# Kernel tuning notes

Measured on AMD Instinct MI355X. Metric: run time of the kernel, lower is better.

Reference implementation:

```python
import jax, jax.numpy as jnp
import numpy as np
from jax import lax

H = 32  # hidden size


def _lstm_layer(x, Wih, Whh, bih, bhh):
    """x: [B, T, D_in]; returns [B, T, H]. PyTorch gate order i,f,g,o."""
    B = x.shape[0]
    b = bih + bhh  # [4H]
    # precompute input projections for all timesteps: [T, B, 4H]
    xp = jnp.einsum('btd,gd->tbg', x, Wih) + b

    def step(carry, xt):
        h, c = carry
        gates = xt + h @ Whh.T  # [B, 4H]
        i, f, g, o = jnp.split(gates, 4, axis=-1)
        i = jax.nn.sigmoid(i)
        f = jax.nn.sigmoid(f)
        g = jnp.tanh(g)
        o = jax.nn.sigmoid(o)
        c = f * c + i * g
        h = o * jnp.tanh(c)
        return (h, c), h

    init = (jnp.zeros((B, H), x.dtype), jnp.zeros((B, H), x.dtype))
    _, ys = lax.scan(step, init, xp)  # ys: [T, B, H]
    return jnp.swapaxes(ys, 0, 1)


def _lstm5(x, Wih0, Wih_rest, Whh, bih, bhh):
    h = _lstm_layer(x, Wih0, Whh[0], bih[0], bhh[0])
    for l in range(4):  # fixed small layer count
        h = _lstm_layer(h, Wih_rest[l], Whh[l + 1], bih[l + 1], bhh[l + 1])
    return h


def setup_inputs() -> dict:
    key = jax.random.key(0)
    ks = jax.random.split(key, 18)
    s = 1.0 / np.sqrt(H)
    B, T = 16384, 20
    u = lambda k, shp: jax.random.uniform(k, shp, jnp.float32, -s, s)
    return {
        'accel': jax.random.normal(ks[0], (B, T, 3), jnp.float32),
        'gyro': jax.random.normal(ks[1], (B, T, 3), jnp.float32),
        'accel_Wih0': u(ks[2], (4 * H, 3)),
        'accel_Wih_rest': u(ks[3], (4, 4 * H, H)),
        'accel_Whh': u(ks[4], (5, 4 * H, H)),
        'accel_bih': u(ks[5], (5, 4 * H)),
        'accel_bhh': u(ks[6], (5, 4 * H)),
        'gyro_Wih0': u(ks[7], (4 * H, 3)),
        'gyro_Wih_rest': u(ks[8], (4, 4 * H, H)),
        'gyro_Whh': u(ks[9], (5, 4 * H, H)),
        'gyro_bih': u(ks[10], (5, 4 * H)),
        'gyro_bhh': u(ks[11], (5, 4 * H)),
        'fc1_w': u(ks[12], (128, T * H * 2)),
        'fc1_b': u(ks[13], (128,)),
        'fc2_w': u(ks[14], (5, 128)),
        'fc2_b': u(ks[15], (5,)),
    }


def reference(accel, gyro, accel_Wih0, accel_Wih_rest, accel_Whh, accel_bih,
              accel_bhh, gyro_Wih0, gyro_Wih_rest, gyro_Whh, gyro_bih,
              gyro_bhh, fc1_w, fc1_b, fc2_w, fc2_b):
    a = _lstm5(accel, accel_Wih0, accel_Wih_rest, accel_Whh, accel_bih, accel_bhh)
    g = _lstm5(gyro, gyro_Wih0, gyro_Wih_rest, gyro_Whh, gyro_bih, gyro_bhh)
    x = jnp.concatenate([a, g], axis=1)          # [B, 2T, H]
    x = x.reshape(x.shape[0], -1)                # [B, 2*T*H]
    x = jax.nn.relu(x @ fc1_w.T + fc1_b)         # [B, 128]
    return x @ fc2_w.T + fc2_b                   # [B, 5]
```

## Files before the change

kernel.cpp:

```cpp
#include <hip/hip_runtime.h>
#include <math.h>

#define B_TOTAL 16384
#define T_STEPS 20
#define NGRP    1024

typedef __attribute__((ext_vector_type(8))) __bf16 bf16x8;
typedef __attribute__((ext_vector_type(4))) float f32x4;

__device__ __forceinline__ __bf16 bf16_bits(unsigned short s) {
    __bf16 r; __builtin_memcpy(&r, &s, 2); return r;
}
__device__ __forceinline__ void split_trunc(float x, __bf16& hi, __bf16& lo) {
    unsigned u = __float_as_uint(x);
    hi = bf16_bits((unsigned short)(u >> 16));
    float l = x - __uint_as_float(u & 0xFFFF0000u);
    lo = bf16_bits((unsigned short)(__float_as_uint(l) >> 16));
}

__device__ __forceinline__ float lstm_act(f32x4 a, float& c) {
    float eA = __expf(-a[0]);
    float eB = __expf(-a[1]);
    float eC = __expf(2.0f * a[2]);
    float aA = 1.0f + eA, aB = 1.0f + eB, aC = 1.0f + eC;
    float pAC = aA * aC;
    float r1  = __builtin_amdgcn_rcpf(pAC * aB);
    c = fmaf(c, pAC, (eC - 1.0f) * aB) * r1;
    float eD = __expf(-a[3]);
    float eE = __expf(2.0f * c);
    float r2 = __builtin_amdgcn_rcpf((1.0f + eD) * (1.0f + eE));
    return (eE - 1.0f) * r2;
}

__global__ __launch_bounds__(512, 8)
void lstm5_mfma(const float* __restrict__ accel, const float* __restrict__ gyro,
                const float* __restrict__ aWih0, const float* __restrict__ aWihR,
                const float* __restrict__ aWhh,  const float* __restrict__ aBih,
                const float* __restrict__ aBhh,
                const float* __restrict__ gWih0, const float* __restrict__ gWihR,
                const float* __restrict__ gWhh,  const float* __restrict__ gBih,
                const float* __restrict__ gBhh,
                __bf16* __restrict__ Xhi, __bf16* __restrict__ Xlo) {
    const int tid  = threadIdx.x;
    const int w    = tid >> 6;
    const int lane = tid & 63;
    const int e    = lane & 15;
    const int quad = lane >> 4;
    const int sensor = blockIdx.y;
    const int bbase  = blockIdx.x * 16;

    const float* xin  = sensor ? gyro  : accel;
    const float* Wih0 = sensor ? gWih0 : aWih0;
    const float* WihR = sensor ? gWihR : aWihR;
    const float* Whh  = sensor ? gWhh  : aWhh;
    const float* Bih  = sensor ? gBih  : aBih;
    const float* Bhh  = sensor ? gBhh  : aBhh;

    __shared__ __align__(16) __bf16 shi[20 * 512];
    __shared__ __align__(16) __bf16 slo[20 * 512];

    const int ug  = w * 4 + quad;
    const int swz = (e >> 1) & 3;

    const int widx = (e * 16 + ((w * 2 + (quad >> 1)) ^ (swz << 2))) * 2 + (quad & 1);
    const int rb_base = e * 32 + ((quad ^ swz) << 3);

    const int m_row = lane & 15;
    const int orow  = (m_row & 3) * 32 + (w * 4 + (m_row >> 2));

    bf16x8 wih_h, wih_l, whh_h, whh_l;
    f32x4  biasv;
    float  c0 = 0.f;

#define LOAD_FRAG(Wsrc, fh, fl)                               \
    {                                                         \
        const float* p_ = (Wsrc) + (orow) * 32 + quad * 8;    \
        _Pragma("unroll")                                     \
        for (int jj = 0; jj < 8; ++jj) {                      \
            __bf16 h_, l_;                                    \
            split_trunc(p_[jj], h_, l_);                      \
            (fh)[jj] = h_;  (fl)[jj] = l_;                    \
        }                                                     \
    }

#define LOAD_BIAS(l)                                                        \
    {                                                                       \
        _Pragma("unroll")                                                   \
        for (int r = 0; r < 4; ++r)                                         \
            biasv[r] = Bih[(l) * 128 + r * 32 + ug] + Bhh[(l) * 128 + r * 32 + ug]; \
    }

#define ACT_STORE(t)                                                        \
    {                                                                       \
        float h0 = lstm_act(acc, c0);                                       \
        __bf16 hh_, ll_;                                                    \
        split_trunc(h0, hh_, ll_);                                          \
        __syncthreads();             \
        shi[(t) * 512 + widx] = hh_;                                        \
        slo[(t) * 512 + widx] = ll_;                                        \
        __syncthreads();       \
    }

    {
        LOAD_FRAG(Whh, whh_h, whh_l);
        LOAD_BIAS(0);
        float w0reg[4][3];
#pragma unroll
        for (int r = 0; r < 4; ++r)
#pragma unroll
            for (int k = 0; k < 3; ++k)
                w0reg[r][k] = Wih0[(r * 32 + ug) * 3 + k];
        const float* xrow = xin + (size_t)(bbase + e) * (T_STEPS * 3);

        for (int t = 0; t < T_STEPS; ++t) {
            float x0 = xrow[t * 3 + 0];
            float x1 = xrow[t * 3 + 1];
            float x2 = xrow[t * 3 + 2];
            f32x4 acc = biasv;
#pragma unroll
            for (int r = 0; r < 4; ++r)
                acc[r] = fmaf(w0reg[r][0], x0,
                         fmaf(w0reg[r][1], x1,
                         fmaf(w0reg[r][2], x2, acc[r])));
            if (t > 0) {
                int rb = (t - 1) * 512 + rb_base;
                bf16x8 bh = *(const bf16x8*)&shi[rb];
                bf16x8 bl = *(const bf16x8*)&slo[rb];
                acc = __builtin_amdgcn_mfma_f32_16x16x32_bf16(whh_h, bh, acc, 0, 0, 0);
                acc = __builtin_amdgcn_mfma_f32_16x16x32_bf16(whh_h, bl, acc, 0, 0, 0);
                acc = __builtin_amdgcn_mfma_f32_16x16x32_bf16(whh_l, bh, acc, 0, 0, 0);
            }
            ACT_STORE(t);
        }
    }

    for (int l = 1; l < 5; ++l) {
        const float* Wi = WihR + (l - 1) * 4096;
        const float* Wh = Whh + l * 4096;
        LOAD_FRAG(Wi, wih_h, wih_l);
        LOAD_FRAG(Wh, whh_h, whh_l);
        LOAD_BIAS(l);
        c0 = 0.f;

        for (int t = 0; t < T_STEPS; ++t) {
            const int rb1 = t * 512 + rb_base;
            bf16x8 bh1 = *(const bf16x8*)&shi[rb1];
            bf16x8 bl1 = *(const bf16x8*)&slo[rb1];
            f32x4 acc;
            acc = __builtin_amdgcn_mfma_f32_16x16x32_bf16(wih_h, bh1, biasv, 0, 0, 0);
            acc = __builtin_amdgcn_mfma_f32_16x16x32_bf16(wih_h, bl1, acc, 0, 0, 0);
            acc = __builtin_amdgcn_mfma_f32_16x16x32_bf16(wih_l, bh1, acc, 0, 0, 0);
            if (t > 0) {
                const int rb0 = rb1 - 512;
                bf16x8 bh = *(const bf16x8*)&shi[rb0];
                bf16x8 bl = *(const bf16x8*)&slo[rb0];
                acc = __builtin_amdgcn_mfma_f32_16x16x32_bf16(whh_h, bh, acc, 0, 0, 0);
                acc = __builtin_amdgcn_mfma_f32_16x16x32_bf16(whh_h, bl, acc, 0, 0, 0);
                acc = __builtin_amdgcn_mfma_f32_16x16x32_bf16(whh_l, bh, acc, 0, 0, 0);
            }
            ACT_STORE(t);
        }
    }
    __syncthreads();

    {
        size_t base = ((size_t)(sensor * NGRP + blockIdx.x)) * (20 * 512);
        float4* dh = (float4*)(Xhi + base);
        float4* dl = (float4*)(Xlo + base);
        const float4* sh = (const float4*)shi;
        const float4* sl = (const float4*)slo;
        for (int i = tid; i < 1280; i += 512) { dh[i] = sh[i]; dl[i] = sl[i]; }
    }
#undef LOAD_FRAG
#undef LOAD_BIAS
#undef ACT_STORE
}

__global__ void w1_prep(const float* __restrict__ w1,
                        __bf16* __restrict__ w1ah, __bf16* __restrict__ w1al) {
    int t = blockIdx.x * blockDim.x + threadIdx.x;
    if (t >= 20480) return;
    int lane = t & 63;
    int ks   = (t >> 6) % 40;
    int mt   = t / (64 * 40);
    int row  = mt * 16 + (lane & 15);
    int col0 = ks * 32 + (lane >> 4) * 8;
    const float* src = w1 + row * 1280 + col0;
#pragma unroll
    for (int j = 0; j < 8; ++j) {
        __bf16 h_, l_;
        split_trunc(src[j], h_, l_);
        w1ah[t * 8 + j] = h_;
        w1al[t * 8 + j] = l_;
    }
}

__global__ __launch_bounds__(256, 4)
void fc_mfma(const __bf16* __restrict__ Xhi, const __bf16* __restrict__ Xlo,
             const __bf16* __restrict__ w1ah, const __bf16* __restrict__ w1al,
             const float* __restrict__ fc1_b, const float* __restrict__ fc2_w,
             const float* __restrict__ fc2_b, float* __restrict__ out) {
    const int tid  = threadIdx.x;
    const int wv   = tid >> 6;
    const int lane = tid & 63;
    const int e    = lane & 15;
    const int quad = lane >> 4;
    const int g    = blockIdx.x;

    const int lnoff = e * 32 + ((quad ^ ((e >> 1) & 3)) << 3);

    __shared__ __align__(16) f32x4 sacc[4][8][64];
    __shared__ float sred[4][16][5];

    f32x4 acc[8];
#pragma unroll
    for (int m = 0; m < 8; ++m) acc[m] = (f32x4){0.f, 0.f, 0.f, 0.f};

    for (int kk = 0; kk < 10; ++kk) {
        int ks = wv * 10 + kk;
        int sensor = ks / 20, t = ks % 20;
        size_t bb = ((size_t)(sensor * NGRP + g)) * (20 * 512) + t * 512 + lnoff;
        bf16x8 bh = *(const bf16x8*)(Xhi + bb);
        bf16x8 bl = *(const bf16x8*)(Xlo + bb);
#pragma unroll
        for (int m = 0; m < 8; ++m) {
            const __bf16* ap = w1ah + ((size_t)((m * 40 + ks) * 64 + lane)) * 8;
            const __bf16* al = w1al + ((size_t)((m * 40 + ks) * 64 + lane)) * 8;
            bf16x8 ah = *(const bf16x8*)ap;
            bf16x8 av = *(const bf16x8*)al;
            acc[m] = __builtin_amdgcn_mfma_f32_16x16x32_bf16(ah, bh, acc[m], 0, 0, 0);
            acc[m] = __builtin_amdgcn_mfma_f32_16x16x32_bf16(ah, bl, acc[m], 0, 0, 0);
            acc[m] = __builtin_amdgcn_mfma_f32_16x16x32_bf16(av, bh, acc[m], 0, 0, 0);
        }
    }
#pragma unroll
    for (int m = 0; m < 8; ++m) sacc[wv][m][lane] = acc[m];
    __syncthreads();

    float p[5] = {0.f, 0.f, 0.f, 0.f, 0.f};
#pragma unroll
    for (int mm = 0; mm < 2; ++mm) {
        int mt = wv * 2 + mm;
        f32x4 z = sacc[0][mt][lane];
#pragma unroll
        for (int k = 1; k < 4; ++k) {
            f32x4 zz = sacc[k][mt][lane];
#pragma unroll
            for (int r = 0; r < 4; ++r) z[r] += zz[r];
        }
#pragma unroll
        for (int r = 0; r < 4; ++r) {
            int row = mt * 16 + quad * 4 + r;
            float v = fmaxf(z[r] + fc1_b[row], 0.f);
#pragma unroll
            for (int n = 0; n < 5; ++n) p[n] = fmaf(v, fc2_w[n * 128 + row], p[n]);
        }
    }
#pragma unroll
    for (int n = 0; n < 5; ++n) {
        p[n] += __shfl_xor(p[n], 16, 64);
        p[n] += __shfl_xor(p[n], 32, 64);
    }
    if (quad == 0) {
#pragma unroll
        for (int n = 0; n < 5; ++n) sred[wv][e][n] = p[n];
    }
    __syncthreads();
    if (tid < 80) {
        int col = tid / 5, n = tid - col * 5;
        out[(size_t)(g * 16 + col) * 5 + n] =
            sred[0][col][n] + sred[1][col][n] + sred[2][col][n] + sred[3][col][n] + fc2_b[n];
    }
}

extern "C" void kernel_launch(void* const* d_in, const int* in_sizes, int n_in,
                              void* d_out, int out_size, void* d_ws, size_t ws_size,
                              hipStream_t stream) {
    const float* accel  = (const float*)d_in[0];
    const float* gyro   = (const float*)d_in[1];
    const float* aWih0  = (const float*)d_in[2];
    const float* aWihR  = (const float*)d_in[3];
    const float* aWhh   = (const float*)d_in[4];
    const float* aBih   = (const float*)d_in[5];
    const float* aBhh   = (const float*)d_in[6];
    const float* gWih0  = (const float*)d_in[7];
    const float* gWihR  = (const float*)d_in[8];
    const float* gWhh   = (const float*)d_in[9];
    const float* gBih   = (const float*)d_in[10];
    const float* gBhh   = (const float*)d_in[11];
    const float* fc1_w  = (const float*)d_in[12];
    const float* fc1_b  = (const float*)d_in[13];
    const float* fc2_w  = (const float*)d_in[14];
    const float* fc2_b  = (const float*)d_in[15];
    float* out = (float*)d_out;

    const size_t XN = (size_t)2 * NGRP * 20 * 512;
    __bf16* Xhi  = (__bf16*)d_ws;
    __bf16* Xlo  = Xhi + XN;
    __bf16* W1ah = Xlo + XN;
    __bf16* W1al = W1ah + 163840;

    hipLaunchKernelGGL(w1_prep, dim3(80), dim3(256), 0, stream, fc1_w, W1ah, W1al);

    hipLaunchKernelGGL(lstm5_mfma, dim3(NGRP, 2), dim3(512), 0, stream,
                       accel, gyro, aWih0, aWihR, aWhh, aBih, aBhh,
                       gWih0, gWihR, gWhh, gBih, gBhh, Xhi, Xlo);

    hipLaunchKernelGGL(fc_mfma, dim3(NGRP), dim3(256), 0, stream,
                       Xhi, Xlo, W1ah, W1al, fc1_b, fc2_w, fc2_b, out);
}
```

Before: 291.2 us.

## Use 2-wave LSTM blocks with four hidden units per lane and packed stores

Each LSTM block shrinks from 8 waves to 2, and each lane now computes four hidden units. Each wave therefore issues four independent MFMA chains per timestep and reuses the same B fragment across them. The hi/lo bf16 halves are packed with a perm instruction and stored as 64-bit words. The goal is to cut the block barrier overhead paid at every timestep and to give each wave more independent work to hide MFMA and transcendental latency. In exchange, register pressure rises (16 weight fragments plus 4 accumulators), the per-timestep activation work is serialized within fewer waves, and launch_bounds now allows fewer resident waves.

```diff
diff --git a/kernel.cpp b/kernel.cpp
--- a/kernel.cpp
+++ b/kernel.cpp
@@ -7,6 +7,14 @@
 
 typedef __attribute__((ext_vector_type(8))) __bf16 bf16x8;
 typedef __attribute__((ext_vector_type(4))) float f32x4;
+
+__device__ __forceinline__ unsigned pack_hi16(unsigned a, unsigned b) {
+#if __has_builtin(__builtin_amdgcn_perm)
+    return __builtin_amdgcn_perm(b, a, 0x07060302u);
+#else
+    return (a >> 16) | (b & 0xFFFF0000u);
+#endif
+}
 
 __device__ __forceinline__ __bf16 bf16_bits(unsigned short s) {
     __bf16 r; __builtin_memcpy(&r, &s, 2); return r;
@@ -32,7 +40,7 @@
     return (eE - 1.0f) * r2;
 }
 
-__global__ __launch_bounds__(512, 8)
+__global__ __launch_bounds__(128, 2)
 void lstm5_mfma(const float* __restrict__ accel, const float* __restrict__ gyro,
                 const float* __restrict__ aWih0, const float* __restrict__ aWihR,
                 const float* __restrict__ aWhh,  const float* __restrict__ aBih,
@@ -56,79 +64,107 @@
     const float* Bih  = sensor ? gBih  : aBih;
     const float* Bhh  = sensor ? gBhh  : aBhh;
 
-    __shared__ __align__(16) __bf16 shi[20 * 512];
-    __shared__ __align__(16) __bf16 slo[20 * 512];
-
-    const int ug  = w * 4 + quad;
+    __shared__ __align__(16) unsigned shi[20 * 256];
+    __shared__ __align__(16) unsigned slo[20 * 256];
+    const __bf16* sh16 = (const __bf16*)shi;
+    const __bf16* sl16 = (const __bf16*)slo;
+
     const int swz = (e >> 1) & 3;
-
-    const int widx = (e * 16 + ((w * 2 + (quad >> 1)) ^ (swz << 2))) * 2 + (quad & 1);
+    const int wr_base = e * 16 + ((w * 8 + quad * 2) ^ (swz << 2));
     const int rb_base = e * 32 + ((quad ^ swz) << 3);
 
-    const int m_row = lane & 15;
-    const int orow  = (m_row & 3) * 32 + (w * 4 + (m_row >> 2));
-
-    bf16x8 wih_h, wih_l, whh_h, whh_l;
-    f32x4  biasv;
-    float  c0 = 0.f;
-
-#define LOAD_FRAG(Wsrc, fh, fl)                               \
-    {                                                         \
-        const float* p_ = (Wsrc) + (orow) * 32 + quad * 8;    \
-        _Pragma("unroll")                                     \
-        for (int jj = 0; jj < 8; ++jj) {                      \
-            __bf16 h_, l_;                                    \
-            split_trunc(p_[jj], h_, l_);                      \
-            (fh)[jj] = h_;  (fl)[jj] = l_;                    \
-        }                                                     \
-    }
-
-#define LOAD_BIAS(l)                                                        \
-    {                                                                       \
-        _Pragma("unroll")                                                   \
-        for (int r = 0; r < 4; ++r)                                         \
-            biasv[r] = Bih[(l) * 128 + r * 32 + ug] + Bhh[(l) * 128 + r * 32 + ug]; \
-    }
-
-#define ACT_STORE(t)                                                        \
-    {                                                                       \
-        float h0 = lstm_act(acc, c0);                                       \
-        __bf16 hh_, ll_;                                                    \
-        split_trunc(h0, hh_, ll_);                                          \
-        __syncthreads();             \
-        shi[(t) * 512 + widx] = hh_;                                        \
-        slo[(t) * 512 + widx] = ll_;                                        \
-        __syncthreads();       \
+    const int orow0 = (e & 3) * 32 + w * 16 + (e >> 2) * 4;
+
+    bf16x8 wih_h[4], wih_l[4], whh_h[4], whh_l[4];
+    f32x4  biasv[4];
+    float  cst[4];
+
+#define LOAD_FRAG(Wsrc, j, fh, fl)                                  \
+    {                                                               \
+        const float* p_ = (Wsrc) + (orow0 + (j)) * 32 + quad * 8;   \
+        _Pragma("unroll")                                           \
+        for (int jj = 0; jj < 8; ++jj) {                            \
+            __bf16 h_, l_;                                          \
+            split_trunc(p_[jj], h_, l_);                            \
+            (fh)[(j)][jj] = h_;  (fl)[(j)][jj] = l_;                \
+        }                                                           \
+    }
+
+#define LOAD_BIAS(l)                                                         \
+    {                                                                        \
+        _Pragma("unroll")                                                    \
+        for (int j = 0; j < 4; ++j) {                                        \
+            int u_ = w * 16 + quad * 4 + j;                                  \
+            _Pragma("unroll")                                                \
+            for (int r = 0; r < 4; ++r)                                      \
+                biasv[j][r] = Bih[(l) * 128 + r * 32 + u_] +                 \
+                              Bhh[(l) * 128 + r * 32 + u_];                  \
+        }                                                                    \
+    }
+
+#define ACT_STORE(t)                                                         \
+    {                                                                        \
+        float h0 = lstm_act(acc[0], cst[0]);                                 \
+        float h1 = lstm_act(acc[1], cst[1]);                                 \
+        float h2 = lstm_act(acc[2], cst[2]);                                 \
+        float h3 = lstm_act(acc[3], cst[3]);                                 \
+        unsigned b0 = __float_as_uint(h0), b1 = __float_as_uint(h1);         \
+        unsigned b2 = __float_as_uint(h2), b3 = __float_as_uint(h3);         \
+        unsigned hw0 = pack_hi16(b0, b1), hw1 = pack_hi16(b2, b3);           \
+        float l0 = h0 - __uint_as_float(b0 & 0xFFFF0000u);                   \
+        float l1 = h1 - __uint_as_float(b1 & 0xFFFF0000u);                   \
+        float l2 = h2 - __uint_as_float(b2 & 0xFFFF0000u);                   \
+        float l3 = h3 - __uint_as_float(b3 & 0xFFFF0000u);                   \
+        unsigned lw0 = pack_hi16(__float_as_uint(l0), __float_as_uint(l1));  \
+        unsigned lw1 = pack_hi16(__float_as_uint(l2), __float_as_uint(l3));  \
+        __syncthreads();              \
+        *(uint2*)(shi + (t) * 256 + wr_base) = make_uint2(hw0, hw1);         \
+        *(uint2*)(slo + (t) * 256 + wr_base) = make_uint2(lw0, lw1);         \
+        __syncthreads();        \
     }
 
     {
-        LOAD_FRAG(Whh, whh_h, whh_l);
+#pragma unroll
+        for (int j = 0; j < 4; ++j) LOAD_FRAG(Whh, j, whh_h, whh_l);
         LOAD_BIAS(0);
-        float w0reg[4][3];
-#pragma unroll
-        for (int r = 0; r < 4; ++r)
-#pragma unroll
-            for (int k = 0; k < 3; ++k)
-                w0reg[r][k] = Wih0[(r * 32 + ug) * 3 + k];
+#pragma unroll
+        for (int j = 0; j < 4; ++j) cst[j] = 0.f;
+
+        float w0reg[4][4][3];
+#pragma unroll
+        for (int j = 0; j < 4; ++j) {
+            int u_ = w * 16 + quad * 4 + j;
+#pragma unroll
+            for (int r = 0; r < 4; ++r)
+#pragma unroll
+                for (int k = 0; k < 3; ++k)
+                    w0reg[j][r][k] = Wih0[(r * 32 + u_) * 3 + k];
+        }
         const float* xrow = xin + (size_t)(bbase + e) * (T_STEPS * 3);
 
         for (int t = 0; t < T_STEPS; ++t) {
             float x0 = xrow[t * 3 + 0];
             float x1 = xrow[t * 3 + 1];
             float x2 = xrow[t * 3 + 2];
-            f32x4 acc = biasv;
-#pragma unroll
-            for (int r = 0; r < 4; ++r)
-                acc[r] = fmaf(w0reg[r][0], x0,
-                         fmaf(w0reg[r][1], x1,
-                         fmaf(w0reg[r][2], x2, acc[r])));
+            f32x4 acc[4];
+#pragma unroll
+            for (int j = 0; j < 4; ++j) {
+#pragma unroll
+                for (int r = 0; r < 4; ++r)
+                    acc[j][r] = fmaf(w0reg[j][r][0], x0,
+                                fmaf(w0reg[j][r][1], x1,
+                                fmaf(w0reg[j][r][2], x2, biasv[j][r])));
+            }
             if (t > 0) {
                 int rb = (t - 1) * 512 + rb_base;
-                bf16x8 bh = *(const bf16x8*)&shi[rb];
-                bf16x8 bl = *(const bf16x8*)&slo[rb];
-                acc = __builtin_amdgcn_mfma_f32_16x16x32_bf16(whh_h, bh, acc, 0, 0, 0);
-                acc = __builtin_amdgcn_mfma_f32_16x16x32_bf16(whh_h, bl, acc, 0, 0, 0);
-                acc = __builtin_amdgcn_mfma_f32_16x16x32_bf16(whh_l, bh, acc, 0, 0, 0);
+                bf16x8 bh = *(const bf16x8*)(sh16 + rb);
+                bf16x8 bl = *(const bf16x8*)(sl16 + rb);
+#pragma unroll
+                for (int j = 0; j < 4; ++j) {
+                    acc[j] = __builtin_amdgcn_mfma_f32_16x16x32_bf16(whh_h[j], bh, acc[j], 0, 0, 0);
+                    acc[j] = __builtin_amdgcn_mfma_f32_16x16x32_bf16(whh_h[j], bl, acc[j], 0, 0, 0);
+                    acc[j] = __builtin_amdgcn_mfma_f32_16x16x32_bf16(whh_l[j], bh, acc[j], 0, 0, 0);
+                }
             }
             ACT_STORE(t);
         }
@@ -137,26 +173,36 @@
     for (int l = 1; l < 5; ++l) {
         const float* Wi = WihR + (l - 1) * 4096;
         const float* Wh = Whh + l * 4096;
-        LOAD_FRAG(Wi, wih_h, wih_l);
-        LOAD_FRAG(Wh, whh_h, whh_l);
+#pragma unroll
+        for (int j = 0; j < 4; ++j) {
+            LOAD_FRAG(Wi, j, wih_h, wih_l);
+            LOAD_FRAG(Wh, j, whh_h, whh_l);
+        }
         LOAD_BIAS(l);
-        c0 = 0.f;
+#pragma unroll
+        for (int j = 0; j < 4; ++j) cst[j] = 0.f;
 
         for (int t = 0; t < T_STEPS; ++t) {
             const int rb1 = t * 512 + rb_base;
-            bf16x8 bh1 = *(const bf16x8*)&shi[rb1];
-            bf16x8 bl1 = *(const bf16x8*)&slo[rb1];
-            f32x4 acc;
-            acc = __builtin_amdgcn_mfma_f32_16x16x32_bf16(wih_h, bh1, biasv, 0, 0, 0);
-            acc = __builtin_amdgcn_mfma_f32_16x16x32_bf16(wih_h, bl1, acc, 0, 0, 0);
-            acc = __builtin_amdgcn_mfma_f32_16x16x32_bf16(wih_l, bh1, acc, 0, 0, 0);
+            bf16x8 bh1 = *(const bf16x8*)(sh16 + rb1);
+            bf16x8 bl1 = *(const bf16x8*)(sl16 + rb1);
+            f32x4 acc[4];
+#pragma unroll
+            for (int j = 0; j < 4; ++j) {
+                acc[j] = __builtin_amdgcn_mfma_f32_16x16x32_bf16(wih_h[j], bh1, biasv[j], 0, 0, 0);
+                acc[j] = __builtin_amdgcn_mfma_f32_16x16x32_bf16(wih_h[j], bl1, acc[j], 0, 0, 0);
+                acc[j] = __builtin_amdgcn_mfma_f32_16x16x32_bf16(wih_l[j], bh1, acc[j], 0, 0, 0);
+            }
             if (t > 0) {
                 const int rb0 = rb1 - 512;
-                bf16x8 bh = *(const bf16x8*)&shi[rb0];
-                bf16x8 bl = *(const bf16x8*)&slo[rb0];
-                acc = __builtin_amdgcn_mfma_f32_16x16x32_bf16(whh_h, bh, acc, 0, 0, 0);
-                acc = __builtin_amdgcn_mfma_f32_16x16x32_bf16(whh_h, bl, acc, 0, 0, 0);
-                acc = __builtin_amdgcn_mfma_f32_16x16x32_bf16(whh_l, bh, acc, 0, 0, 0);
+                bf16x8 bh = *(const bf16x8*)(sh16 + rb0);
+                bf16x8 bl = *(const bf16x8*)(sl16 + rb0);
+#pragma unroll
+                for (int j = 0; j < 4; ++j) {
+                    acc[j] = __builtin_amdgcn_mfma_f32_16x16x32_bf16(whh_h[j], bh, acc[j], 0, 0, 0);
+                    acc[j] = __builtin_amdgcn_mfma_f32_16x16x32_bf16(whh_h[j], bl, acc[j], 0, 0, 0);
+                    acc[j] = __builtin_amdgcn_mfma_f32_16x16x32_bf16(whh_l[j], bh, acc[j], 0, 0, 0);
+                }
             }
             ACT_STORE(t);
         }
@@ -169,7 +215,7 @@
         float4* dl = (float4*)(Xlo + base);
         const float4* sh = (const float4*)shi;
         const float4* sl = (const float4*)slo;
-        for (int i = tid; i < 1280; i += 512) { dh[i] = sh[i]; dl[i] = sl[i]; }
+        for (int i = tid; i < 1280; i += 128) { dh[i] = sh[i]; dl[i] = sl[i]; }
     }
 #undef LOAD_FRAG
 #undef LOAD_BIAS
@@ -302,7 +348,7 @@
 
     hipLaunchKernelGGL(w1_prep, dim3(80), dim3(256), 0, stream, fc1_w, W1ah, W1al);
 
-    hipLaunchKernelGGL(lstm5_mfma, dim3(NGRP, 2), dim3(512), 0, stream,
+    hipLaunchKernelGGL(lstm5_mfma, dim3(NGRP, 2), dim3(128), 0, stream,
                        accel, gyro, aWih0, aWihR, aWhh, aBih, aBhh,
                        gWih0, gWihR, gWhh, gBih, gBhh, Xhi, Xlo);
 
```

New measurement: 317.1 us. 1.09x slower.

## Use ring buffer of LDS slabs to drop one barrier per LSTM step

Applied to the files above, without the earlier changes.

Shared hidden-state storage becomes a 21-slab ring buffer, so each layer writes to a fresh slab rather than overwriting the one other waves may still be reading. This removes the pre-write __syncthreads and leaves one barrier per timestep. The input-projection operand for the next step is now loaded before the barrier, overlapping the LDS read with the sync. It adds modular index arithmetic, uses about 5% more LDS, and lowers the launch-bounds occupancy hint from 8 to 6, which may change register allocation.

```diff
diff --git a/kernel.cpp b/kernel.cpp
--- a/kernel.cpp
+++ b/kernel.cpp
@@ -4,6 +4,7 @@
 #define B_TOTAL 16384
 #define T_STEPS 20
 #define NGRP    1024
+#define NSLAB   21
 
 typedef __attribute__((ext_vector_type(8))) __bf16 bf16x8;
 typedef __attribute__((ext_vector_type(4))) float f32x4;
@@ -32,7 +33,7 @@
     return (eE - 1.0f) * r2;
 }
 
-__global__ __launch_bounds__(512, 8)
+__global__ __launch_bounds__(512, 6)
 void lstm5_mfma(const float* __restrict__ accel, const float* __restrict__ gyro,
                 const float* __restrict__ aWih0, const float* __restrict__ aWihR,
                 const float* __restrict__ aWhh,  const float* __restrict__ aBih,
@@ -56,8 +57,8 @@
     const float* Bih  = sensor ? gBih  : aBih;
     const float* Bhh  = sensor ? gBhh  : aBhh;
 
-    __shared__ __align__(16) __bf16 shi[20 * 512];
-    __shared__ __align__(16) __bf16 slo[20 * 512];
+    __shared__ __align__(16) __bf16 shi[NSLAB * 512];
+    __shared__ __align__(16) __bf16 slo[NSLAB * 512];
 
     const int ug  = w * 4 + quad;
     const int swz = (e >> 1) & 3;
@@ -90,17 +91,6 @@
             biasv[r] = Bih[(l) * 128 + r * 32 + ug] + Bhh[(l) * 128 + r * 32 + ug]; \
     }
 
-#define ACT_STORE(t)                                                        \
-    {                                                                       \
-        float h0 = lstm_act(acc, c0);                                       \
-        __bf16 hh_, ll_;                                                    \
-        split_trunc(h0, hh_, ll_);                                          \
-        __syncthreads();             \
-        shi[(t) * 512 + widx] = hh_;                                        \
-        slo[(t) * 512 + widx] = ll_;                                        \
-        __syncthreads();       \
-    }
-
     {
         LOAD_FRAG(Whh, whh_h, whh_l);
         LOAD_BIAS(0);
@@ -112,6 +102,7 @@
                 w0reg[r][k] = Wih0[(r * 32 + ug) * 3 + k];
         const float* xrow = xin + (size_t)(bbase + e) * (T_STEPS * 3);
 
+        int sw = 0;
         for (int t = 0; t < T_STEPS; ++t) {
             float x0 = xrow[t * 3 + 0];
             float x1 = xrow[t * 3 + 1];
@@ -123,14 +114,21 @@
                          fmaf(w0reg[r][1], x1,
                          fmaf(w0reg[r][2], x2, acc[r])));
             if (t > 0) {
-                int rb = (t - 1) * 512 + rb_base;
+                int s_hh = sw - 1; if (s_hh < 0) s_hh += NSLAB;
+                int rb = s_hh * 512 + rb_base;
                 bf16x8 bh = *(const bf16x8*)&shi[rb];
                 bf16x8 bl = *(const bf16x8*)&slo[rb];
                 acc = __builtin_amdgcn_mfma_f32_16x16x32_bf16(whh_h, bh, acc, 0, 0, 0);
                 acc = __builtin_amdgcn_mfma_f32_16x16x32_bf16(whh_h, bl, acc, 0, 0, 0);
                 acc = __builtin_amdgcn_mfma_f32_16x16x32_bf16(whh_l, bh, acc, 0, 0, 0);
             }
-            ACT_STORE(t);
+            float h0 = lstm_act(acc, c0);
+            __bf16 hh_, ll_;
+            split_trunc(h0, hh_, ll_);
+            shi[sw * 512 + widx] = hh_;
+            slo[sw * 512 + widx] = ll_;
+            __syncthreads();
+            ++sw; if (sw >= NSLAB) sw -= NSLAB;
         }
     }
 
@@ -142,23 +140,42 @@
         LOAD_BIAS(l);
         c0 = 0.f;
 
+        int sw = NSLAB - l;
+        bf16x8 ih_h, ih_l;
+        {
+            int s_ih = sw + 1; if (s_ih >= NSLAB) s_ih -= NSLAB;
+            int rb = s_ih * 512 + rb_base;
+            ih_h = *(const bf16x8*)&shi[rb];
+            ih_l = *(const bf16x8*)&slo[rb];
+        }
+
         for (int t = 0; t < T_STEPS; ++t) {
-            const int rb1 = t * 512 + rb_base;
-            bf16x8 bh1 = *(const bf16x8*)&shi[rb1];
-            bf16x8 bl1 = *(const bf16x8*)&slo[rb1];
             f32x4 acc;
-            acc = __builtin_amdgcn_mfma_f32_16x16x32_bf16(wih_h, bh1, biasv, 0, 0, 0);
-            acc = __builtin_amdgcn_mfma_f32_16x16x32_bf16(wih_h, bl1, acc, 0, 0, 0);
-            acc = __builtin_amdgcn_mfma_f32_16x16x32_bf16(wih_l, bh1, acc, 0, 0, 0);
+            acc = __builtin_amdgcn_mfma_f32_16x16x32_bf16(wih_h, ih_h, biasv, 0, 0, 0);
+            acc = __builtin_amdgcn_mfma_f32_16x16x32_bf16(wih_h, ih_l, acc, 0, 0, 0);
+            acc = __builtin_amdgcn_mfma_f32_16x16x32_bf16(wih_l, ih_h, acc, 0, 0, 0);
             if (t > 0) {
-                const int rb0 = rb1 - 512;
-                bf16x8 bh = *(const bf16x8*)&shi[rb0];
-                bf16x8 bl = *(const bf16x8*)&slo[rb0];
+                int s_hh = sw - 1; if (s_hh < 0) s_hh += NSLAB;
+                int rb = s_hh * 512 + rb_base;
+                bf16x8 bh = *(const bf16x8*)&shi[rb];
+                bf16x8 bl = *(const bf16x8*)&slo[rb];
                 acc = __builtin_amdgcn_mfma_f32_16x16x32_bf16(whh_h, bh, acc, 0, 0, 0);
                 acc = __builtin_amdgcn_mfma_f32_16x16x32_bf16(whh_h, bl, acc, 0, 0, 0);
                 acc = __builtin_amdgcn_mfma_f32_16x16x32_bf16(whh_l, bh, acc, 0, 0, 0);
             }
-            ACT_STORE(t);
+            float h0 = lstm_act(acc, c0);
+            __bf16 hh_, ll_;
+            split_trunc(h0, hh_, ll_);
+            shi[sw * 512 + widx] = hh_;
+            slo[sw * 512 + widx] = ll_;
+            {
+                int s_pf = sw + 2; if (s_pf >= NSLAB) s_pf -= NSLAB;
+                int rb = s_pf * 512 + rb_base;
+                ih_h = *(const bf16x8*)&shi[rb];
+                ih_l = *(const bf16x8*)&slo[rb];
+            }
+            __syncthreads();
+            ++sw; if (sw >= NSLAB) sw -= NSLAB;
         }
     }
     __syncthreads();
@@ -169,11 +186,16 @@
         float4* dl = (float4*)(Xlo + base);
         const float4* sh = (const float4*)shi;
         const float4* sl = (const float4*)slo;
-        for (int i = tid; i < 1280; i += 512) { dh[i] = sh[i]; dl[i] = sl[i]; }
+        for (int i = tid; i < 1280; i += 512) {
+            int tl   = i >> 6;
+            int phys = tl + 17; if (phys >= NSLAB) phys -= NSLAB;
+            int off  = i & 63;
+            dh[i] = sh[phys * 64 + off];
+            dl[i] = sl[phys * 64 + off];
+        }
     }
 #undef LOAD_FRAG
 #undef LOAD_BIAS
-#undef ACT_STORE
 }
 
 __global__ void w1_prep(const float* __restrict__ w1,
```

Measured after the change: 309.1 us. +6.1%, slower.

## Fold exp scaling into weights, halve barriers, prefetch next-step input in LSTM

Applied to the files above, without the earlier changes.

Pre-scales the gate weights and biases by log2(e), or 2·log2(e) for the g gate, so activations can use raw exp2 and skip a multiply per exponential. Each step now uses one __syncthreads instead of two, made safe by prefetching the next timestep's input fragment into registers before the in-place store. The layer-1..4 time loop is fully unrolled. This relies on the register-held previous-layer input being read before it is overwritten, and it raises register pressure and code size.

```diff
diff --git a/kernel.cpp b/kernel.cpp
--- a/kernel.cpp
+++ b/kernel.cpp
@@ -7,6 +7,17 @@
 
 typedef __attribute__((ext_vector_type(8))) __bf16 bf16x8;
 typedef __attribute__((ext_vector_type(4))) float f32x4;
+
+#define LOG2E_F 1.4426950408889634f
+#define K2_F    2.8853900817779268f
+
+__device__ __forceinline__ float exp2_fast(float x) {
+#if __has_builtin(__builtin_amdgcn_exp2f)
+    return __builtin_amdgcn_exp2f(x);
+#else
+    return __expf(x * 0.6931471805599453f);
+#endif
+}
 
 __device__ __forceinline__ __bf16 bf16_bits(unsigned short s) {
     __bf16 r; __builtin_memcpy(&r, &s, 2); return r;
@@ -18,16 +29,16 @@
     lo = bf16_bits((unsigned short)(__float_as_uint(l) >> 16));
 }
 
-__device__ __forceinline__ float lstm_act(f32x4 a, float& c) {
-    float eA = __expf(-a[0]);
-    float eB = __expf(-a[1]);
-    float eC = __expf(2.0f * a[2]);
+__device__ __forceinline__ float lstm_act2(f32x4 a, float& c) {
+    float eA = exp2_fast(-a[0]);
+    float eB = exp2_fast(-a[1]);
+    float eC = exp2_fast(a[2]);
     float aA = 1.0f + eA, aB = 1.0f + eB, aC = 1.0f + eC;
     float pAC = aA * aC;
     float r1  = __builtin_amdgcn_rcpf(pAC * aB);
     c = fmaf(c, pAC, (eC - 1.0f) * aB) * r1;
-    float eD = __expf(-a[3]);
-    float eE = __expf(2.0f * c);
+    float eD = exp2_fast(-a[3]);
+    float eE = exp2_fast(K2_F * c);
     float r2 = __builtin_amdgcn_rcpf((1.0f + eD) * (1.0f + eE));
     return (eE - 1.0f) * r2;
 }
@@ -56,8 +67,8 @@
     const float* Bih  = sensor ? gBih  : aBih;
     const float* Bhh  = sensor ? gBhh  : aBhh;
 
-    __shared__ __align__(16) __bf16 shi[20 * 512];
-    __shared__ __align__(16) __bf16 slo[20 * 512];
+    __shared__ __align__(16) __bf16 shi[T_STEPS * 512];
+    __shared__ __align__(16) __bf16 slo[T_STEPS * 512];
 
     const int ug  = w * 4 + quad;
     const int swz = (e >> 1) & 3;
@@ -67,8 +78,10 @@
 
     const int m_row = lane & 15;
     const int orow  = (m_row & 3) * 32 + (w * 4 + (m_row >> 2));
+    const float wscale = ((m_row & 3) == 2) ? K2_F : LOG2E_F;
 
     bf16x8 wih_h, wih_l, whh_h, whh_l;
+    bf16x8 ih_h, ih_l;
     f32x4  biasv;
     float  c0 = 0.f;
 
@@ -78,7 +91,7 @@
         _Pragma("unroll")                                     \
         for (int jj = 0; jj < 8; ++jj) {                      \
             __bf16 h_, l_;                                    \
-            split_trunc(p_[jj], h_, l_);                      \
+            split_trunc(p_[jj] * wscale, h_, l_);             \
             (fh)[jj] = h_;  (fl)[jj] = l_;                    \
         }                                                     \
     }
@@ -86,19 +99,11 @@
 #define LOAD_BIAS(l)                                                        \
     {                                                                       \
         _Pragma("unroll")                                                   \
-        for (int r = 0; r < 4; ++r)                                         \
-            biasv[r] = Bih[(l) * 128 + r * 32 + ug] + Bhh[(l) * 128 + r * 32 + ug]; \
-    }
-
-#define ACT_STORE(t)                                                        \
-    {                                                                       \
-        float h0 = lstm_act(acc, c0);                                       \
-        __bf16 hh_, ll_;                                                    \
-        split_trunc(h0, hh_, ll_);                                          \
-        __syncthreads();             \
-        shi[(t) * 512 + widx] = hh_;                                        \
-        slo[(t) * 512 + widx] = ll_;                                        \
-        __syncthreads();       \
+        for (int r = 0; r < 4; ++r) {                                       \
+            float bs_ = (r == 2) ? K2_F : LOG2E_F;                          \
+            biasv[r] = (Bih[(l) * 128 + r * 32 + ug] +                      \
+                        Bhh[(l) * 128 + r * 32 + ug]) * bs_;                \
+        }                                                                   \
     }
 
     {
@@ -106,10 +111,12 @@
         LOAD_BIAS(0);
         float w0reg[4][3];
 #pragma unroll
-        for (int r = 0; r < 4; ++r)
+        for (int r = 0; r < 4; ++r) {
+            float bs_ = (r == 2) ? K2_F : LOG2E_F;
 #pragma unroll
             for (int k = 0; k < 3; ++k)
-                w0reg[r][k] = Wih0[(r * 32 + ug) * 3 + k];
+                w0reg[r][k] = Wih0[(r * 32 + ug) * 3 + k] * bs_;
+        }
         const float* xrow = xin + (size_t)(bbase + e) * (T_STEPS * 3);
 
         for (int t = 0; t < T_STEPS; ++t) {
@@ -130,8 +137,42 @@
                 acc = __builtin_amdgcn_mfma_f32_16x16x32_bf16(whh_h, bl, acc, 0, 0, 0);
                 acc = __builtin_amdgcn_mfma_f32_16x16x32_bf16(whh_l, bh, acc, 0, 0, 0);
             }
-            ACT_STORE(t);
-        }
+            float h0 = lstm_act2(acc, c0);
+            __bf16 hh_, ll_;
+            split_trunc(h0, hh_, ll_);
+            shi[t * 512 + widx] = hh_;
+            slo[t * 512 + widx] = ll_;
+            __syncthreads();
+        }
+    }
+
+#define STEP_L(t)                                                           \
+    {                                                                       \
+        bf16x8 bh, bl, pf_h, pf_l;                                          \
+        if ((t) > 0) {                                                      \
+            bh = *(const bf16x8*)&shi[((t) - 1) * 512 + rb_base];           \
+            bl = *(const bf16x8*)&slo[((t) - 1) * 512 + rb_base];           \
+        }                                                                   \
+        if ((t) < T_STEPS - 1) {               \
+            pf_h = *(const bf16x8*)&shi[((t) + 1) * 512 + rb_base];         \
+            pf_l = *(const bf16x8*)&slo[((t) + 1) * 512 + rb_base];         \
+        }                                                                   \
+        f32x4 acc;                                                          \
+        acc = __builtin_amdgcn_mfma_f32_16x16x32_bf16(wih_h, ih_h, biasv, 0, 0, 0); \
+        acc = __builtin_amdgcn_mfma_f32_16x16x32_bf16(wih_h, ih_l, acc, 0, 0, 0);   \
+        acc = __builtin_amdgcn_mfma_f32_16x16x32_bf16(wih_l, ih_h, acc, 0, 0, 0);   \
+        if ((t) > 0) {                                                      \
+            acc = __builtin_amdgcn_mfma_f32_16x16x32_bf16(whh_h, bh, acc, 0, 0, 0); \
+            acc = __builtin_amdgcn_mfma_f32_16x16x32_bf16(whh_h, bl, acc, 0, 0, 0); \
+            acc = __builtin_amdgcn_mfma_f32_16x16x32_bf16(whh_l, bh, acc, 0, 0, 0); \
+        }                                                                   \
+        float h0 = lstm_act2(acc, c0);                                      \
+        __bf16 hh_, ll_;                                                    \
+        split_trunc(h0, hh_, ll_);                                          \
+        shi[(t) * 512 + widx] = hh_;                                        \
+        slo[(t) * 512 + widx] = ll_;                                        \
+        if ((t) < T_STEPS - 1) { ih_h = pf_h; ih_l = pf_l; }                \
+        __syncthreads();                 \
     }
 
     for (int l = 1; l < 5; ++l) {
@@ -142,24 +183,12 @@
         LOAD_BIAS(l);
         c0 = 0.f;
 
-        for (int t = 0; t < T_STEPS; ++t) {
-            const int rb1 = t * 512 + rb_base;
-            bf16x8 bh1 = *(const bf16x8*)&shi[rb1];
-            bf16x8 bl1 = *(const bf16x8*)&slo[rb1];
-            f32x4 acc;
-            acc = __builtin_amdgcn_mfma_f32_16x16x32_bf16(wih_h, bh1, biasv, 0, 0, 0);
-            acc = __builtin_amdgcn_mfma_f32_16x16x32_bf16(wih_h, bl1, acc, 0, 0, 0);
-            acc = __builtin_amdgcn_mfma_f32_16x16x32_bf16(wih_l, bh1, acc, 0, 0, 0);
-            if (t > 0) {
-                const int rb0 = rb1 - 512;
-                bf16x8 bh = *(const bf16x8*)&shi[rb0];
-                bf16x8 bl = *(const bf16x8*)&slo[rb0];
-                acc = __builtin_amdgcn_mfma_f32_16x16x32_bf16(whh_h, bh, acc, 0, 0, 0);
-                acc = __builtin_amdgcn_mfma_f32_16x16x32_bf16(whh_h, bl, acc, 0, 0, 0);
-                acc = __builtin_amdgcn_mfma_f32_16x16x32_bf16(whh_l, bh, acc, 0, 0, 0);
-            }
-            ACT_STORE(t);
-        }
+        ih_h = *(const bf16x8*)&shi[rb_base];
+        ih_l = *(const bf16x8*)&slo[rb_base];
+        __syncthreads();
+
+#pragma unroll
+        for (int t = 0; t < T_STEPS; ++t) STEP_L(t);
     }
     __syncthreads();
 
@@ -173,7 +202,7 @@
     }
 #undef LOAD_FRAG
 #undef LOAD_BIAS
-#undef ACT_STORE
+#undef STEP_L
 }
 
 __global__ void w1_prep(const float* __restrict__ w1,
```

New measurement: 285.7 us. Within noise of the previous version (-1.9%).
